# Performance work log

Hardware: AMD Instinct MI355X
Metric: run time of the kernel (lower is better)

## Reference

```python
import jax, jax.numpy as jnp
import numpy as np

B, CIN, COUT, K, H, W = 4, 16, 16, 3, 128, 128


def setup_inputs() -> dict:
    key = jax.random.key(0)
    k1, k2, k3 = jax.random.split(key, 3)
    x = jax.random.normal(k1, (B, CIN, H, W), dtype=jnp.float32)
    # kaiming_uniform_(a=1.0): bound = sqrt(6 / ((1 + a^2) * fan_in)), fan_in = Cin*k*k
    fan_in = CIN * K * K
    bound = float(np.sqrt(6.0 / (2.0 * fan_in)))
    weights = jax.random.uniform(k2, (H, W, COUT, CIN, K, K), dtype=jnp.float32,
                                 minval=-bound, maxval=bound)
    bias = jax.random.normal(k3, (H, W, COUT), dtype=jnp.float32)
    return {"x": x, "weights": weights, "bias": bias}


def _xonv2d(x, weights, bias):
    b, c, h, w = x.shape
    k = weights.shape[-1]
    pad = k // 2
    if k % 2 == 1:
        xp = jnp.pad(x, ((0, 0), (0, 0), (pad, pad), (pad, pad)))
    else:
        xp = jnp.pad(x, ((0, 0), (0, 0), (pad - 1, pad), (pad - 1, pad)))
    # Unfold: patch element order matches torch view -> (c, kh, kw) flattened.
    # Stack k*k shifted views: (B, C, k*k, H, W)
    shifts = [xp[:, :, i:i + h, j:j + w] for i in range(k) for j in range(k)]
    patches = jnp.stack(shifts, axis=2)
    wflat = weights.reshape(h, w, weights.shape[2], c, k * k)  # (H,W,O,C,p)
    # out[b,o,h,w] = sum_{c,p} patches[b,c,p,h,w] * wflat[h,w,o,c,p]
    out = jnp.einsum('bcphw,hwocp->bohw', patches, wflat)
    out = out + jnp.transpose(bias, (2, 0, 1))[None]  # (1,O,H,W)
    return out


def reference(x, weights, bias):
    return _xonv2d(x, weights, bias)
```

## Files before the change

kernel.cpp:

```cpp
#include <hip/hip_runtime.h>


#define HWD   128
#define CIND  16
#define COUTD 16
#define BATCH 4
#define SPW   4
#define WPB   4

typedef float f4  __attribute__((ext_vector_type(4)));
typedef float f4u __attribute__((ext_vector_type(4), aligned(4)));

__device__ __forceinline__ void gload_lds16(const f4* gsrc, f4* ldst) {
    __builtin_amdgcn_global_load_lds(
        (const __attribute__((address_space(1))) unsigned int*)gsrc,
        (__attribute__((address_space(3))) unsigned int*)ldst,
        16, 0, 0);
}

__global__ __launch_bounds__(256) void xonv2d_kernel(
    const float* __restrict__ x,
    const float* __restrict__ wts,
    const float* __restrict__ bias,
    float* __restrict__ out)
{
    __shared__ f4 wbuf[WPB][576];
    __shared__ f4 xslot[WPB][192];

    const int lane = threadIdx.x & 63;
    const int wave = threadIdx.x >> 6;

    const int xcd = blockIdx.x & 7;
    const int idx = blockIdx.x >> 3;
    const int site0 = xcd * 2048 + (idx * WPB + wave) * SPW;

    const int o  = lane & 15;
    const int g  = lane >> 4;
    const int c0 = g * 4;

    int sb[3], sc[3], sr[3];
    #pragma unroll
    for (int j = 0; j < 3; ++j) {
        const int S = lane + 64 * j;
        sb[j] = S / 48;
        const int u = S - sb[j] * 48;
        sc[j] = u / 3;
        sr[j] = u - sc[j] * 3;
    }

    {
        const f4* gw = (const f4*)wts + (size_t)site0 * 576;
        #pragma unroll
        for (int j = 0; j < 9; ++j)
            gload_lds16(gw + j * 64 + lane, &wbuf[wave][j * 64]);
    }

    #pragma unroll 1
    for (int s = 0; s < SPW; ++s) {
        const int site = site0 + s;
        const int h = site >> 7;
        const int w = site & 127;

        if (s == 0) asm volatile("s_waitcnt vmcnt(0)" ::: "memory");
        else        asm volatile("s_waitcnt vmcnt(1)" ::: "memory");
        __builtin_amdgcn_sched_barrier(0);

        f4 wv[9];
        {
            const f4* lp = &wbuf[wave][o * 36 + g * 9];
            #pragma unroll
            for (int j = 0; j < 9; ++j) wv[j] = lp[j];
        }
        asm volatile("s_waitcnt lgkmcnt(0)" ::: "memory");
        __builtin_amdgcn_sched_barrier(0);
        const float* wf = (const float*)wv;

        f4 xr[3];
        const bool wfast = (w >= 1) && (w <= HWD - 3);
        #pragma unroll
        for (int j = 0; j < 3; ++j) {
            const int hy  = h + sr[j] - 1;
            const bool okh = (unsigned)hy < (unsigned)HWD;
            const int hyc = okh ? hy : 0;
            const float* xb = x + ((size_t)(sb[j] * CIND + sc[j]) * HWD + hyc) * HWD;
            if (wfast) {
                f4 v = *(const f4u*)(xb + (w - 1));
                xr[j] = okh ? v : (f4){0.f, 0.f, 0.f, 0.f};
            } else {
                f4 v;
                #pragma unroll
                for (int jj = 0; jj < 4; ++jj) {
                    const int cw = w - 1 + jj;
                    const bool ok = okh && ((unsigned)cw < (unsigned)HWD);
                    v[jj] = ok ? xb[cw] : 0.f;
                }
                xr[j] = v;
            }
        }
        const float bv = bias[(size_t)site * COUTD + o];
        __builtin_amdgcn_sched_barrier(0);

        if (s + 1 < SPW) {
            const f4* gw = (const f4*)wts + (size_t)(site + 1) * 576;
            #pragma unroll
            for (int j = 0; j < 9; ++j)
                gload_lds16(gw + j * 64 + lane, &wbuf[wave][j * 64]);
        }
        __builtin_amdgcn_sched_barrier(0);

        if (s + 1 < SPW) asm volatile("s_waitcnt vmcnt(9)" ::: "memory");
        else             asm volatile("s_waitcnt vmcnt(0)" ::: "memory");
        __builtin_amdgcn_sched_barrier(0);

        #pragma unroll
        for (int j = 0; j < 3; ++j)
            xslot[wave][lane + 64 * j] = xr[j];

        float acc[BATCH] = {0.f, 0.f, 0.f, 0.f};
        #pragma unroll
        for (int cc = 0; cc < 4; ++cc) {
            #pragma unroll
            for (int b = 0; b < BATCH; ++b) {
                const f4* xp = &xslot[wave][(b * CIND + c0 + cc) * 3];
                const f4 r0 = xp[0];
                const f4 r1 = xp[1];
                const f4 r2 = xp[2];
                const float* wr = wf + cc * 9;
                acc[b] = fmaf(r0.x, wr[0], acc[b]);
                acc[b] = fmaf(r0.y, wr[1], acc[b]);
                acc[b] = fmaf(r0.z, wr[2], acc[b]);
                acc[b] = fmaf(r1.x, wr[3], acc[b]);
                acc[b] = fmaf(r1.y, wr[4], acc[b]);
                acc[b] = fmaf(r1.z, wr[5], acc[b]);
                acc[b] = fmaf(r2.x, wr[6], acc[b]);
                acc[b] = fmaf(r2.y, wr[7], acc[b]);
                acc[b] = fmaf(r2.z, wr[8], acc[b]);
            }
        }

        float r[BATCH];
        #pragma unroll
        for (int b = 0; b < BATCH; ++b) {
            float v = acc[b];
            v += __shfl_xor(v, 32);
            v += __shfl_xor(v, 16);
            r[b] = v;
        }

        const float vout = (g == 0) ? r[0] : (g == 1) ? r[1] : (g == 2) ? r[2] : r[3];
        out[((size_t)(g * COUTD + o)) * (HWD * HWD) + h * HWD + w] = vout + bv;
    }
}

extern "C" void kernel_launch(void* const* d_in, const int* in_sizes, int n_in,
                              void* d_out, int out_size, void* d_ws, size_t ws_size,
                              hipStream_t stream) {
    const float* x    = (const float*)d_in[0];
    const float* wts  = (const float*)d_in[1];
    const float* bias = (const float*)d_in[2];
    float* out = (float*)d_out;

    const int blocks = (HWD * HWD) / (WPB * SPW);
    xonv2d_kernel<<<blocks, WPB * 64, 0, stream>>>(x, wts, bias, out);
}
```

Measured before the change: 240.6 us.

## Replace LDS-direct weight loads with register double-buffered prefetch two sites ahead

Weights are no longer loaded with global_load_lds straight into LDS. They are now read into two register staging sets (stA/stB), prefetched two sites ahead, and written to LDS by each wave before the transposed read-back. The site loop is fully unrolled through a helper, and the explicit vmcnt waits are dropped in favour of compiler-managed waits. The aim is deeper prefetch so the weight stream stays in flight longer, at the cost of about 72 extra VGPRs for staging, possible occupancy loss, and an extra LDS write per site.

```diff
diff --git a/kernel.cpp b/kernel.cpp
--- a/kernel.cpp
+++ b/kernel.cpp
@@ -11,11 +11,108 @@
 typedef float f4  __attribute__((ext_vector_type(4)));
 typedef float f4u __attribute__((ext_vector_type(4), aligned(4)));
 
-__device__ __forceinline__ void gload_lds16(const f4* gsrc, f4* ldst) {
-    __builtin_amdgcn_global_load_lds(
-        (const __attribute__((address_space(1))) unsigned int*)gsrc,
-        (__attribute__((address_space(3))) unsigned int*)ldst,
-        16, 0, 0);
+struct WaveCtx {
+    const float* x;
+    const float* bias;
+    float*       out;
+    const f4*    gw0;
+    f4*          wbuf;
+    f4*          xslot;
+    int site0, lane, o, g;
+    int sb[3], sc[3], sr[3];
+};
+
+__device__ __forceinline__ void site_iter(const WaveCtx& W, const int s,
+                                          f4 (&st)[9], const bool burst)
+{
+    const int site = W.site0 + s;
+    const int h = site >> 7;
+    const int w = site & 127;
+
+    #pragma unroll
+    for (int j = 0; j < 9; ++j)
+        W.wbuf[j * 64 + W.lane] = st[j];
+    f4 wv[9];
+    {
+        const f4* lp = W.wbuf + (W.o * 36 + W.g * 9);
+        #pragma unroll
+        for (int j = 0; j < 9; ++j) wv[j] = lp[j];
+    }
+    const float* wf = (const float*)wv;
+    __builtin_amdgcn_sched_barrier(0);
+
+    f4 xr[3];
+    const bool wfast = (w >= 1) && (w <= HWD - 3);
+    #pragma unroll
+    for (int j = 0; j < 3; ++j) {
+        const int hy   = h + W.sr[j] - 1;
+        const bool okh = (unsigned)hy < (unsigned)HWD;
+        const int hyc  = okh ? hy : 0;
+        const float* xb = W.x + ((size_t)(W.sb[j] * CIND + W.sc[j]) * HWD + hyc) * HWD;
+        if (wfast) {
+            f4 v = *(const f4u*)(xb + (w - 1));
+            xr[j] = okh ? v : (f4){0.f, 0.f, 0.f, 0.f};
+        } else {
+            f4 v;
+            #pragma unroll
+            for (int jj = 0; jj < 4; ++jj) {
+                const int cw = w - 1 + jj;
+                const bool ok = okh && ((unsigned)cw < (unsigned)HWD);
+                v[jj] = ok ? xb[cw] : 0.f;
+            }
+            xr[j] = v;
+        }
+    }
+    const float bv = W.bias[(size_t)site * COUTD + W.o];
+    __builtin_amdgcn_sched_barrier(0);
+
+    if (burst) {
+        const f4* gw = W.gw0 + (size_t)(s + 2) * 576;
+        #pragma unroll
+        for (int j = 0; j < 9; ++j)
+            st[j] = gw[j * 64 + W.lane];
+    }
+    __builtin_amdgcn_sched_barrier(0);
+
+    #pragma unroll
+    for (int j = 0; j < 3; ++j)
+        W.xslot[W.lane + 64 * j] = xr[j];
+
+    const int c0 = W.g * 4;
+    float acc[BATCH] = {0.f, 0.f, 0.f, 0.f};
+    #pragma unroll
+    for (int cc = 0; cc < 4; ++cc) {
+        #pragma unroll
+        for (int b = 0; b < BATCH; ++b) {
+            const f4* xp = &W.xslot[(b * CIND + c0 + cc) * 3];
+            const f4 r0 = xp[0];
+            const f4 r1 = xp[1];
+            const f4 r2 = xp[2];
+            const float* wr = wf + cc * 9;
+            acc[b] = fmaf(r0.x, wr[0], acc[b]);
+            acc[b] = fmaf(r0.y, wr[1], acc[b]);
+            acc[b] = fmaf(r0.z, wr[2], acc[b]);
+            acc[b] = fmaf(r1.x, wr[3], acc[b]);
+            acc[b] = fmaf(r1.y, wr[4], acc[b]);
+            acc[b] = fmaf(r1.z, wr[5], acc[b]);
+            acc[b] = fmaf(r2.x, wr[6], acc[b]);
+            acc[b] = fmaf(r2.y, wr[7], acc[b]);
+            acc[b] = fmaf(r2.z, wr[8], acc[b]);
+        }
+    }
+
+    float r[BATCH];
+    #pragma unroll
+    for (int b = 0; b < BATCH; ++b) {
+        float v = acc[b];
+        v += __shfl_xor(v, 32);
+        v += __shfl_xor(v, 16);
+        r[b] = v;
+    }
+
+    const float vout = (W.g == 0) ? r[0] : (W.g == 1) ? r[1] : (W.g == 2) ? r[2] : r[3];
+    W.out[((size_t)(W.g * COUTD + W.o)) * (HWD * HWD) + h * HWD + w] = vout + bv;
+    __builtin_amdgcn_sched_barrier(0);
 }
 
 __global__ __launch_bounds__(256) void xonv2d_kernel(
@@ -34,122 +131,36 @@
     const int idx = blockIdx.x >> 3;
     const int site0 = xcd * 2048 + (idx * WPB + wave) * SPW;
 
-    const int o  = lane & 15;
-    const int g  = lane >> 4;
-    const int c0 = g * 4;
+    WaveCtx W;
+    W.x = x; W.bias = bias; W.out = out;
+    W.gw0   = (const f4*)wts + (size_t)site0 * 576;
+    W.wbuf  = wbuf[wave];
+    W.xslot = xslot[wave];
+    W.site0 = site0;
+    W.lane  = lane;
+    W.o     = lane & 15;
+    W.g     = lane >> 4;
 
-    int sb[3], sc[3], sr[3];
     #pragma unroll
     for (int j = 0; j < 3; ++j) {
         const int S = lane + 64 * j;
-        sb[j] = S / 48;
-        const int u = S - sb[j] * 48;
-        sc[j] = u / 3;
-        sr[j] = u - sc[j] * 3;
+        W.sb[j] = S / 48;
+        const int u = S - W.sb[j] * 48;
+        W.sc[j] = u / 3;
+        W.sr[j] = u - W.sc[j] * 3;
     }
 
-    {
-        const f4* gw = (const f4*)wts + (size_t)site0 * 576;
-        #pragma unroll
-        for (int j = 0; j < 9; ++j)
-            gload_lds16(gw + j * 64 + lane, &wbuf[wave][j * 64]);
-    }
+    f4 stA[9], stB[9];
+    #pragma unroll
+    for (int j = 0; j < 9; ++j) stA[j] = W.gw0[j * 64 + lane];
+    #pragma unroll
+    for (int j = 0; j < 9; ++j) stB[j] = W.gw0[576 + j * 64 + lane];
+    __builtin_amdgcn_sched_barrier(0);
 
-    #pragma unroll 1
-    for (int s = 0; s < SPW; ++s) {
-        const int site = site0 + s;
-        const int h = site >> 7;
-        const int w = site & 127;
-
-        if (s == 0) asm volatile("s_waitcnt vmcnt(0)" ::: "memory");
-        else        asm volatile("s_waitcnt vmcnt(1)" ::: "memory");
-        __builtin_amdgcn_sched_barrier(0);
-
-        f4 wv[9];
-        {
-            const f4* lp = &wbuf[wave][o * 36 + g * 9];
-            #pragma unroll
-            for (int j = 0; j < 9; ++j) wv[j] = lp[j];
-        }
-        asm volatile("s_waitcnt lgkmcnt(0)" ::: "memory");
-        __builtin_amdgcn_sched_barrier(0);
-        const float* wf = (const float*)wv;
-
-        f4 xr[3];
-        const bool wfast = (w >= 1) && (w <= HWD - 3);
-        #pragma unroll
-        for (int j = 0; j < 3; ++j) {
-            const int hy  = h + sr[j] - 1;
-            const bool okh = (unsigned)hy < (unsigned)HWD;
-            const int hyc = okh ? hy : 0;
-            const float* xb = x + ((size_t)(sb[j] * CIND + sc[j]) * HWD + hyc) * HWD;
-            if (wfast) {
-                f4 v = *(const f4u*)(xb + (w - 1));
-                xr[j] = okh ? v : (f4){0.f, 0.f, 0.f, 0.f};
-            } else {
-                f4 v;
-                #pragma unroll
-                for (int jj = 0; jj < 4; ++jj) {
-                    const int cw = w - 1 + jj;
-                    const bool ok = okh && ((unsigned)cw < (unsigned)HWD);
-                    v[jj] = ok ? xb[cw] : 0.f;
-                }
-                xr[j] = v;
-            }
-        }
-        const float bv = bias[(size_t)site * COUTD + o];
-        __builtin_amdgcn_sched_barrier(0);
-
-        if (s + 1 < SPW) {
-            const f4* gw = (const f4*)wts + (size_t)(site + 1) * 576;
-            #pragma unroll
-            for (int j = 0; j < 9; ++j)
-                gload_lds16(gw + j * 64 + lane, &wbuf[wave][j * 64]);
-        }
-        __builtin_amdgcn_sched_barrier(0);
-
-        if (s + 1 < SPW) asm volatile("s_waitcnt vmcnt(9)" ::: "memory");
-        else             asm volatile("s_waitcnt vmcnt(0)" ::: "memory");
-        __builtin_amdgcn_sched_barrier(0);
-
-        #pragma unroll
-        for (int j = 0; j < 3; ++j)
-            xslot[wave][lane + 64 * j] = xr[j];
-
-        float acc[BATCH] = {0.f, 0.f, 0.f, 0.f};
-        #pragma unroll
-        for (int cc = 0; cc < 4; ++cc) {
-            #pragma unroll
-            for (int b = 0; b < BATCH; ++b) {
-                const f4* xp = &xslot[wave][(b * CIND + c0 + cc) * 3];
-                const f4 r0 = xp[0];
-                const f4 r1 = xp[1];
-                const f4 r2 = xp[2];
-                const float* wr = wf + cc * 9;
-                acc[b] = fmaf(r0.x, wr[0], acc[b]);
-                acc[b] = fmaf(r0.y, wr[1], acc[b]);
-                acc[b] = fmaf(r0.z, wr[2], acc[b]);
-                acc[b] = fmaf(r1.x, wr[3], acc[b]);
-                acc[b] = fmaf(r1.y, wr[4], acc[b]);
-                acc[b] = fmaf(r1.z, wr[5], acc[b]);
-                acc[b] = fmaf(r2.x, wr[6], acc[b]);
-                acc[b] = fmaf(r2.y, wr[7], acc[b]);
-                acc[b] = fmaf(r2.z, wr[8], acc[b]);
-            }
-        }
-
-        float r[BATCH];
-        #pragma unroll
-        for (int b = 0; b < BATCH; ++b) {
-            float v = acc[b];
-            v += __shfl_xor(v, 32);
-            v += __shfl_xor(v, 16);
-            r[b] = v;
-        }
-
-        const float vout = (g == 0) ? r[0] : (g == 1) ? r[1] : (g == 2) ? r[2] : r[3];
-        out[((size_t)(g * COUTD + o)) * (HWD * HWD) + h * HWD + w] = vout + bv;
-    }
+    site_iter(W, 0, stA, true);
+    site_iter(W, 1, stB, true);
+    site_iter(W, 2, stA, false);
+    site_iter(W, 3, stB, false);
 }
 
 extern "C" void kernel_launch(void* const* d_in, const int* in_sizes, int n_in,
```

Result: faster. 233.4 us (-3.0%).
